# Kernel tuning notes

Measured on AMD Instinct MI355X. Metric: run time of the kernel, lower is better.

Reference implementation:

```python
import jax, jax.numpy as jnp
import numpy as np

NUM_ENTITIES = 100000
NUM_TIMES = 10000
D = 512
DB = 768
NUM_REL = 200
NUM_BASES = 4
N_NODES = 30000
N_EDGES = 200000
B = 128
P_ENT = 64
P_TIME = 32
T_UNIQ = 2000


def setup_inputs() -> dict:
    key = jax.random.key(0)
    ks = jax.random.split(key, 32)
    n = jax.random.normal
    ri = jax.random.randint
    inp = {}
    # learned params
    inp['emb'] = n(ks[0], (NUM_ENTITIES + NUM_TIMES, D), jnp.float32) * 0.05
    sc = 1.0 / np.sqrt(D)
    inp['basis1'] = n(ks[1], (NUM_BASES, D, D), jnp.float32) * sc
    inp['att1'] = n(ks[2], (NUM_REL, NUM_BASES), jnp.float32) * 0.5
    inp['root1'] = n(ks[3], (D, D), jnp.float32) * sc
    inp['bias1'] = jnp.zeros((D,), jnp.float32)
    inp['basis2'] = n(ks[4], (NUM_BASES, D, D), jnp.float32) * sc
    inp['att2'] = n(ks[5], (NUM_REL, NUM_BASES), jnp.float32) * 0.5
    inp['root2'] = n(ks[6], (D, D), jnp.float32) * sc
    inp['bias2'] = jnp.zeros((D,), jnp.float32)
    sb = 1.0 / np.sqrt(DB)
    inp['W_lin'] = n(ks[7], (DB, D), jnp.float32) * sb
    inp['b_lin'] = jnp.zeros((D,), jnp.float32)
    inp['W_attn'] = n(ks[8], (DB, D), jnp.float32) * sb
    inp['b_attn'] = jnp.zeros((D,), jnp.float32)
    inp['W_prob'] = n(ks[9], (DB, 1), jnp.float32) * sb
    inp['b_prob'] = jnp.zeros((1,), jnp.float32)
    # forward tensor args
    inp['ques_emb_bert'] = n(ks[10], (B, DB), jnp.float32)
    inp['x_idx'] = ri(ks[11], (N_NODES,), 0, NUM_ENTITIES, jnp.int32)
    inp['edge_index'] = ri(ks[12], (2, N_EDGES), 0, N_NODES, jnp.int32)
    inp['edge_type'] = ri(ks[13], (N_EDGES,), 0, NUM_REL, jnp.int32)
    inp['start_time'] = ri(ks[14], (N_EDGES,), 0, NUM_TIMES, jnp.int32)
    inp['end_time'] = ri(ks[15], (N_EDGES,), 0, NUM_TIMES, jnp.int32)
    inp['edge_batch_idx'] = jnp.sort(ri(ks[16], (N_EDGES,), 0, B, jnp.int32))
    inp['edge_norm'] = jax.random.uniform(ks[17], (N_EDGES,), jnp.float32)
    inp['uniq_times'] = ri(ks[18], (T_UNIQ,), 0, NUM_TIMES, jnp.int32)
    # padded index vectors: positions >= count point at the appended zero row
    ent_counts = ri(ks[19], (B,), 1, P_ENT + 1, jnp.int32)
    time_counts = ri(ks[20], (B,), 1, P_TIME + 1, jnp.int32)
    pe = ri(ks[21], (B, P_ENT), 0, N_NODES, jnp.int32)
    pt = ri(ks[22], (B, P_TIME), 0, T_UNIQ, jnp.int32)
    inp['padded_ent'] = jnp.where(jnp.arange(P_ENT)[None, :] < ent_counts[:, None], pe, N_NODES)
    inp['padded_time'] = jnp.where(jnp.arange(P_TIME)[None, :] < time_counts[:, None], pt, T_UNIQ)
    inp['ent_counts'] = ent_counts
    inp['time_counts'] = time_counts
    return inp


def rgcn_layer(x, basis, att, root, bias, src, dst, etype, st_emb, et_emb, q_t, edge_norm):
    # basis decomposition: project all nodes through each basis once. [N, NB, D]
    xb = jnp.einsum('ni,bio->nbo', x, basis)
    coeff = att[etype]                                 # [E, NB]
    msg = jnp.einsum('eb,ebd->ed', coeff, xb[src])     # [E, D]
    # time gate: question-time embedding vs edge interval midpoint embedding
    gate = jax.nn.sigmoid(jnp.sum(q_t * 0.5 * (st_emb + et_emb), axis=-1))  # [E]
    msg = msg * (gate * edge_norm)[:, None]
    agg = jax.ops.segment_sum(msg, dst, num_segments=N_NODES)
    return agg + x @ root + bias


def reference(emb, basis1, att1, root1, bias1, basis2, att2, root2, bias2,
              W_lin, b_lin, W_attn, b_attn, W_prob, b_prob,
              ques_emb_bert, x_idx, edge_index, edge_type, start_time, end_time,
              edge_batch_idx, edge_norm, uniq_times, padded_ent, padded_time,
              ent_counts, time_counts):
    question_embedding = ques_emb_bert @ W_lin + b_lin                  # [B, D]
    time_for_edge_attn = (ques_emb_bert @ W_attn + b_attn)[edge_batch_idx]  # [E, D]
    st_emb = emb[start_time + NUM_ENTITIES]
    et_emb = emb[end_time + NUM_ENTITIES]
    x = emb[x_idx]                                                      # [N, D]
    src, dst = edge_index[0], edge_index[1]
    h = jax.nn.relu(rgcn_layer(x, basis1, att1, root1, bias1, src, dst, edge_type,
                               st_emb, et_emb, time_for_edge_attn, edge_norm))
    # dropout is identity in eval mode
    h = rgcn_layer(h, basis2, att2, root2, bias2, src, dst, edge_type,
                   st_emb, et_emb, time_for_edge_attn, edge_norm)       # [N, D]
    subgraph_time_emb = emb[uniq_times + NUM_ENTITIES]                  # [T_u, D]
    zero = jnp.zeros((1, D), h.dtype)
    ent_w_zeros = jnp.concatenate([h, zero], axis=0)
    time_w_zeros = jnp.concatenate([subgraph_time_emb, zero], axis=0)
    pooled_ent = jnp.sum(ent_w_zeros[padded_ent], axis=1) / ent_counts[:, None].astype(h.dtype)
    pooled_time = jnp.sum(time_w_zeros[padded_time], axis=1) / time_counts[:, None].astype(h.dtype)
    p_ent = jax.nn.sigmoid(ques_emb_bert @ W_prob + b_prob)             # [B, 1]
    pred = (question_embedding + pooled_ent * p_ent + pooled_time * (1.0 - p_ent)) / 3.0
    # batched cosine similarity against full entity+time vocab
    pred_n = pred / jnp.maximum(jnp.linalg.norm(pred, axis=-1, keepdims=True), 1e-8)
    emb_n = emb / jnp.maximum(jnp.linalg.norm(emb, axis=-1, keepdims=True), 1e-8)
    score = pred_n @ emb_n.T                                            # [B, V]
    return score * 30.0
```

## Files before the change

kernel.cpp:

```cpp
#include <hip/hip_runtime.h>

#define NUM_ENT   100000
#define NTIMES    10000
#define DD        512
#define DB        768
#define NREL      200
#define NBAS      4
#define NN        30000
#define NEDGE     200000
#define BATCH     128
#define PENT      64
#define PTIME     32
#define TUNIQ     2000
#define V_TOT     110000
#define V_PAD     110208
#define VT16      6888
#define M_PAD2    30208
#define MT2R      1888
#define KT_L      80
#define KT_E      16

typedef __attribute__((ext_vector_type(8))) short s8v;
typedef __attribute__((ext_vector_type(4))) float f4v;

__device__ __forceinline__ unsigned short f2bf(float x){
  unsigned int u = __builtin_bit_cast(unsigned int, x);
  u += 0x7fffu + ((u >> 16) & 1u);
  return (unsigned short)(u >> 16);
}
__device__ __forceinline__ float bf2f(unsigned short h){
  unsigned int u = ((unsigned int)h) << 16;
  return __builtin_bit_cast(float, u);
}

__device__ __forceinline__ void gload16(const void* g, void* l){
  __builtin_amdgcn_global_load_lds(
      (const __attribute__((address_space(1))) void*)g,
      (__attribute__((address_space(3))) void*)l, 16, 0, 0);
}


__global__ __launch_bounds__(256) void k_conv_emb(const float* __restrict__ emb,
    unsigned short* __restrict__ Bp, float* __restrict__ invn){
  int vt = blockIdx.x;
  int wid = threadIdx.x >> 6, lane = threadIdx.x & 63;
  int vrow = vt * 16 + (lane & 15);
  float ss = 0.f;
  __shared__ float ssw[4][16];
  for (int i = 0; i < 4; ++i){
    int kt = wid + i * 4;
    int k0 = kt * 32 + (lane >> 4) * 8;
    s8v o;
    if (vrow < V_TOT){
      const float4* p = reinterpret_cast<const float4*>(emb + (size_t)vrow * DD + k0);
      float4 v0 = p[0], v1 = p[1];
      ss += v0.x*v0.x + v0.y*v0.y + v0.z*v0.z + v0.w*v0.w;
      ss += v1.x*v1.x + v1.y*v1.y + v1.z*v1.z + v1.w*v1.w;
      o[0] = (short)f2bf(v0.x); o[1] = (short)f2bf(v0.y);
      o[2] = (short)f2bf(v0.z); o[3] = (short)f2bf(v0.w);
      o[4] = (short)f2bf(v1.x); o[5] = (short)f2bf(v1.y);
      o[6] = (short)f2bf(v1.z); o[7] = (short)f2bf(v1.w);
    } else {
      #pragma unroll
      for (int j = 0; j < 8; ++j) o[j] = 0;
    }
    *reinterpret_cast<s8v*>(Bp + ((size_t)(kt * VT16 + vt) << 9) + lane * 8) = o;
  }
  ss += __shfl_xor(ss, 16);
  ss += __shfl_xor(ss, 32);
  if ((lane >> 4) == 0) ssw[wid][lane] = ss;
  __syncthreads();
  if (threadIdx.x < 16){
    float s = ssw[0][threadIdx.x] + ssw[1][threadIdx.x] + ssw[2][threadIdx.x] + ssw[3][threadIdx.x];
    int v = vt * 16 + threadIdx.x;
    invn[v] = (v < V_TOT) ? (1.0f / fmaxf(sqrtf(s), 1e-8f)) : 0.0f;
  }
}

__global__ __launch_bounds__(256) void k_small2(const float* __restrict__ ques,
    const float* __restrict__ Wl, const float* __restrict__ bl,
    const float* __restrict__ Wa, const float* __restrict__ ba,
    const float* __restrict__ Wp, const float* __restrict__ bp,
    float* __restrict__ qlin, float* __restrict__ qattn, float* __restrict__ pent){
  if (blockIdx.x == 32){
    int b = threadIdx.x >> 1, half = threadIdx.x & 1;
    float a = 0.f;
    int k0 = half * 384;
    for (int k = k0; k < k0 + 384; ++k)
      a = fmaf(ques[(size_t)b * DB + k], Wp[k], a);
    a += __shfl_xor(a, 1);
    if (half == 0) pent[b] = 1.f / (1.f + expf(-(a + bp[0])));
    return;
  }
  __shared__ float sq[128 * 96];
  int col = threadIdx.x & 31, bg = threadIdx.x >> 5;
  int c0 = blockIdx.x * 32;
  const float* W = (c0 < 512) ? Wl : Wa;
  int wcol = (c0 & 511) + col;
  float acc[16] = {};
  for (int k0 = 0; k0 < DB; k0 += 96){
    __syncthreads();
    for (int i = threadIdx.x; i < 128 * 96; i += 256){
      int b = i / 96, kk = i - b * 96;
      sq[i] = ques[(size_t)b * DB + k0 + kk];
    }
    __syncthreads();
    for (int kk = 0; kk < 96; kk += 4){
      float w0 = W[(size_t)(k0 + kk + 0) * 512 + wcol];
      float w1 = W[(size_t)(k0 + kk + 1) * 512 + wcol];
      float w2 = W[(size_t)(k0 + kk + 2) * 512 + wcol];
      float w3 = W[(size_t)(k0 + kk + 3) * 512 + wcol];
      #pragma unroll
      for (int bb = 0; bb < 16; ++bb){
        float4 qv = *reinterpret_cast<const float4*>(&sq[(bg * 16 + bb) * 96 + kk]);
        acc[bb] = fmaf(qv.x, w0, fmaf(qv.y, w1, fmaf(qv.z, w2, fmaf(qv.w, w3, acc[bb]))));
      }
    }
  }
  float* dst = (c0 < 512) ? qlin : qattn;
  const float* bias = (c0 < 512) ? bl : ba;
  #pragma unroll
  for (int bb = 0; bb < 16; ++bb)
    dst[(size_t)(bg * 16 + bb) * 512 + wcol] = acc[bb] + bias[wcol];
}

__global__ __launch_bounds__(256) void k_pack_qrows(const float* __restrict__ src,
    unsigned short* __restrict__ Ap){
  int w = (int)((blockIdx.x * 256 + threadIdx.x) >> 6);
  int lane = threadIdx.x & 63;
  if (w >= BATCH) return;
  const float* p = src + (size_t)w * 512 + lane * 8;
  s8v o;
  #pragma unroll
  for (int j = 0; j < 8; ++j) o[j] = (short)f2bf(p[j]);
  *reinterpret_cast<s8v*>(Ap + ((size_t)((w >> 4) * KT_E + (lane >> 2)) << 9)
                             + ((w & 15) + (lane & 3) * 16) * 8) = o;
}

__global__ __launch_bounds__(256) void k_pack_B(const float* __restrict__ basis,
    const float* __restrict__ root, unsigned short* __restrict__ Bp){
  int idx = blockIdx.x * 256 + threadIdx.x;
  if (idx >= KT_L * 32 * 64) return;
  int lane = idx & 63; int kt = idx >> 11;
  int k0 = kt * 32 + (lane >> 4) * 8;
  int col = ((idx >> 6) & 31) * 16 + (lane & 15);
  s8v o;
  #pragma unroll
  for (int j = 0; j < 8; ++j){
    int k = k0 + j;
    float v = (k < 2048) ? basis[(size_t)k * 512 + col] : root[(size_t)(k - 2048) * 512 + col];
    o[j] = (short)f2bf(v);
  }
  *reinterpret_cast<s8v*>(Bp + (size_t)idx * 8) = o;
}

__global__ __launch_bounds__(256) void k_gemm_m2(
    const unsigned short* __restrict__ A, const unsigned short* __restrict__ B,
    float* __restrict__ outf){
  __shared__ __align__(1024) short sAll[3 * 8192];
  const int Kt = KT_E;
  int tid = threadIdx.x;
  int lane = tid & 63, wid = tid >> 6;
  int wr = wid >> 1, wc = wid & 1;
  int rt0 = blockIdx.x * 8;
  int ct0 = blockIdx.y * 8;
  const unsigned short* pA0 = A + ((size_t)(rt0 + 2 * wid) * Kt) * 512 + lane * 8;
  const unsigned short* pA1 = pA0 + (size_t)Kt * 512;
  const unsigned short* pB0 = B + (size_t)(ct0 + 2 * wid) * 512 + lane * 8;
  const unsigned short* pB1 = pB0 + 512;
  size_t gbs = (size_t)VT16 * 512;
  int so = 2 * wid * 512;
  f4v acc[4][4] = {};

  auto STAGE = [&](int buf, int kt){
    short* b = &sAll[buf * 8192];
    gload16(pA0 + (size_t)kt * 512, b + so);
    gload16(pA1 + (size_t)kt * 512, b + so + 512);
    gload16(pB0 + (size_t)kt * gbs, b + 4096 + so);
    gload16(pB1 + (size_t)kt * gbs, b + 4096 + so + 512);
  };
  auto COMPUTE = [&](int buf){
    const short* base = &sAll[buf * 8192];
    s8v af[4], bfr[4];
    #pragma unroll
    for (int m = 0; m < 4; ++m) af[m] = *reinterpret_cast<const s8v*>(base + (wr * 4 + m) * 512 + lane * 8);
    #pragma unroll
    for (int n = 0; n < 4; ++n) bfr[n] = *reinterpret_cast<const s8v*>(base + 4096 + (wc * 4 + n) * 512 + lane * 8);
    #pragma unroll
    for (int m = 0; m < 4; ++m)
      #pragma unroll
      for (int n = 0; n < 4; ++n)
        acc[m][n] = __builtin_amdgcn_mfma_f32_16x16x32_bf16(af[m], bfr[n], acc[m][n], 0, 0, 0);
  };

  STAGE(0, 0);
  STAGE(1, 1);
  int cb = 0, sb = 2;
  for (int kt = 0; kt < Kt - 2; ++kt){
    STAGE(sb, kt + 2);
    asm volatile("s_waitcnt vmcnt(8)" ::: "memory");
    __builtin_amdgcn_s_barrier();
    __builtin_amdgcn_sched_barrier(0);
    COMPUTE(cb);
    __builtin_amdgcn_s_barrier();
    cb = (cb == 2) ? 0 : cb + 1;
    sb = (sb == 2) ? 0 : sb + 1;
  }
  asm volatile("s_waitcnt vmcnt(4)" ::: "memory");
  __builtin_amdgcn_s_barrier();
  __builtin_amdgcn_sched_barrier(0);
  COMPUTE(cb);
  cb = (cb == 2) ? 0 : cb + 1;
  asm volatile("s_waitcnt vmcnt(0)" ::: "memory");
  __builtin_amdgcn_s_barrier();
  __builtin_amdgcn_sched_barrier(0);
  COMPUTE(cb);

  #pragma unroll
  for (int m = 0; m < 4; ++m)
    #pragma unroll
    for (int n = 0; n < 4; ++n){
      int row0 = rt0 * 16 + (wr * 4 + m) * 16 + ((lane >> 4) * 4);
      int col  = (ct0 + wc * 4 + n) * 16 + (lane & 15);
      #pragma unroll
      for (int r = 0; r < 4; ++r){
        int rr = row0 + r;
        if (col < NTIMES) outf[(size_t)rr * NTIMES + col] = acc[m][n][r];
      }
    }
}

__global__ __launch_bounds__(256, 3) void k_score_p(
    const unsigned short* __restrict__ Apred, const unsigned short* __restrict__ Bp,
    const float* __restrict__ invn, float* __restrict__ out){
  __shared__ __align__(1024) short sAll[3 * 8192];
  const int Kt = KT_E;
  int tid = threadIdx.x;
  int lane = tid & 63, wid = tid >> 6;
  int wr = wid >> 1, wc = wid & 1;
  int kq = lane >> 4, r16 = lane & 15;
  int ct0 = blockIdx.x * 8;
  const unsigned short* pA0 = Apred + ((size_t)(2 * wid) * Kt) * 512 + lane * 8;
  const unsigned short* pA1 = pA0 + (size_t)Kt * 512;
  const unsigned short* pB0 = Bp + (size_t)(ct0 + 2 * wid) * 512 + lane * 8;
  const unsigned short* pB1 = pB0 + 512;
  size_t gbs = (size_t)VT16 * 512;
  int so = 2 * wid * 512;
  f4v acc[4][4] = {};

  auto STAGE = [&](int buf, int kt){
    short* b = &sAll[buf * 8192];
    gload16(pA0 + (size_t)kt * 512, b + so);
    gload16(pA1 + (size_t)kt * 512, b + so + 512);
    gload16(pB0 + (size_t)kt * gbs, b + 4096 + so);
    gload16(pB1 + (size_t)kt * gbs, b + 4096 + so + 512);
  };
  auto COMPUTE = [&](int buf){
    const short* base = &sAll[buf * 8192];
    s8v af[4], bfr[4];
    #pragma unroll
    for (int m = 0; m < 4; ++m) af[m] = *reinterpret_cast<const s8v*>(base + (wr * 4 + m) * 512 + lane * 8);
    #pragma unroll
    for (int n = 0; n < 4; ++n) bfr[n] = *reinterpret_cast<const s8v*>(base + 4096 + (wc * 4 + n) * 512 + lane * 8);
    #pragma unroll
    for (int m = 0; m < 4; ++m)
      #pragma unroll
      for (int n = 0; n < 4; ++n)
        acc[m][n] = __builtin_amdgcn_mfma_f32_16x16x32_bf16(af[m], bfr[n], acc[m][n], 0, 0, 0);
  };

  STAGE(0, 0);
  STAGE(1, 1);
  int cb = 0, sb = 2;
  for (int kt = 0; kt < Kt - 2; ++kt){
    STAGE(sb, kt + 2);
    asm volatile("s_waitcnt vmcnt(8)" ::: "memory");
    __builtin_amdgcn_s_barrier();
    __builtin_amdgcn_sched_barrier(0);
    COMPUTE(cb);
    __builtin_amdgcn_s_barrier();
    cb = (cb == 2) ? 0 : cb + 1;
    sb = (sb == 2) ? 0 : sb + 1;
  }
  asm volatile("s_waitcnt vmcnt(4)" ::: "memory");
  __builtin_amdgcn_s_barrier();
  __builtin_amdgcn_sched_barrier(0);
  COMPUTE(cb);
  cb = (cb == 2) ? 0 : cb + 1;
  asm volatile("s_waitcnt vmcnt(0)" ::: "memory");
  __builtin_amdgcn_s_barrier();
  __builtin_amdgcn_sched_barrier(0);
  COMPUTE(cb);

  __syncthreads();
  float* scratch = reinterpret_cast<float*>(sAll) + wid * 2176;
  int colg = ct0 * 16 + wc * 64 + r16 * 4;
  bool c_ok = colg < V_TOT;
  float4 inv4 = float4{0.f, 0.f, 0.f, 0.f};
  if (c_ok){
    inv4 = *reinterpret_cast<const float4*>(invn + colg);
    inv4.x *= 30.f; inv4.y *= 30.f; inv4.z *= 30.f; inv4.w *= 30.f;
  }
  #pragma unroll
  for (int p = 0; p < 2; ++p){
    #pragma unroll
    for (int mm = 0; mm < 2; ++mm){
      int m = p * 2 + mm;
      #pragma unroll
      for (int n = 0; n < 4; ++n)
        #pragma unroll
        for (int r = 0; r < 4; ++r)
          scratch[(mm * 16 + kq * 4 + r) * 68 + n * 16 + r16] = acc[m][n][r];
    }
    #pragma unroll
    for (int i = 0; i < 8; ++i){
      int row_r = i * 4 + kq;
      float4 v = *reinterpret_cast<const float4*>(scratch + row_r * 68 + r16 * 4);
      if (c_ok){
        float4 o;
        o.x = v.x * inv4.x; o.y = v.y * inv4.y; o.z = v.z * inv4.z; o.w = v.w * inv4.w;
        int grr = wr * 64 + p * 32 + row_r;
        *reinterpret_cast<float4*>(out + (size_t)grr * V_TOT + colg) = o;
      }
    }
  }
}

template<int MODE>
__global__ __launch_bounds__(512, 4) void k_gemm256(
    const unsigned short* __restrict__ A, const unsigned short* __restrict__ B,
    const float* __restrict__ bias, unsigned short* __restrict__ outh){
  __shared__ __align__(1024) short sAll[3 * 12288];
  const int Kt = KT_L;
  int tid = threadIdx.x;
  int lane = tid & 63, wid = tid >> 6;
  int wr = wid >> 1, wc = wid & 1;
  int g = blockIdx.x;
  int ng = (g & 7) * 59 + (g >> 3);
  int blkM = ng >> 2, blkN = ng & 3;
  int rt0 = blkM * 16;
  int ct0 = blkN * 8;
  const unsigned short* pA0 = A + ((size_t)(rt0 + wid) * Kt) * 512 + lane * 8;
  const unsigned short* pA1 = A + ((size_t)(rt0 + 8 + wid) * Kt) * 512 + lane * 8;
  const unsigned short* pB0 = B + (size_t)(ct0 + wid) * 512 + lane * 8;
  const size_t gbs = 32 * 512;
  int soA0 = wid * 512, soA1 = (8 + wid) * 512, soB = 8192 + wid * 512;
  f4v acc[4][4] = {};

  auto STAGE = [&](int buf, int kt){
    short* b = &sAll[buf * 12288];
    gload16(pA0 + (size_t)kt * 512, b + soA0);
    gload16(pA1 + (size_t)kt * 512, b + soA1);
    gload16(pB0 + (size_t)kt * gbs, b + soB);
  };
  auto COMPUTE = [&](int buf){
    const short* base = &sAll[buf * 12288];
    s8v af[4], bfr[4];
    #pragma unroll
    for (int m = 0; m < 4; ++m) af[m] = *reinterpret_cast<const s8v*>(base + (wr * 4 + m) * 512 + lane * 8);
    #pragma unroll
    for (int n = 0; n < 4; ++n) bfr[n] = *reinterpret_cast<const s8v*>(base + 8192 + (wc * 4 + n) * 512 + lane * 8);
    __builtin_amdgcn_s_setprio(1);
    #pragma unroll
    for (int m = 0; m < 4; ++m)
      #pragma unroll
      for (int n = 0; n < 4; ++n)
        acc[m][n] = __builtin_amdgcn_mfma_f32_16x16x32_bf16(af[m], bfr[n], acc[m][n], 0, 0, 0);
    __builtin_amdgcn_s_setprio(0);
  };

  STAGE(0, 0);
  STAGE(1, 1);
  int cb = 0, sb = 2;
  for (int kt = 0; kt < Kt - 2; ++kt){
    STAGE(sb, kt + 2);
    asm volatile("s_waitcnt vmcnt(6)" ::: "memory");
    __builtin_amdgcn_s_barrier();
    __builtin_amdgcn_sched_barrier(0);
    COMPUTE(cb);
    __builtin_amdgcn_s_barrier();
    cb = (cb == 2) ? 0 : cb + 1;
    sb = (sb == 2) ? 0 : sb + 1;
  }
  asm volatile("s_waitcnt vmcnt(3)" ::: "memory");
  __builtin_amdgcn_s_barrier();
  __builtin_amdgcn_sched_barrier(0);
  COMPUTE(cb);
  cb = (cb == 2) ? 0 : cb + 1;
  asm volatile("s_waitcnt vmcnt(0)" ::: "memory");
  __builtin_amdgcn_s_barrier();
  __builtin_amdgcn_sched_barrier(0);
  COMPUTE(cb);

  int R0 = blkM * 256 + wr * 64 + (lane >> 4) * 4;
  int C0 = blkN * 128 + wc * 64 + (lane & 15);
  #pragma unroll
  for (int m = 0; m < 4; ++m)
    #pragma unroll
    for (int r4 = 0; r4 < 4; ++r4){
      int rr = R0 + m * 16 + r4;
      if (rr < NN){
        #pragma unroll
        for (int n = 0; n < 4; ++n){
          int col = C0 + n * 16;
          float v = acc[m][n][r4] + bias[col];
          if constexpr (MODE == 1) v = fmaxf(v, 0.f);
          outh[(size_t)rr * 512 + col] = f2bf(v);
        }
      }
    }
}

__global__ __launch_bounds__(256) void k_edgeprep(const int* __restrict__ ebatch,
    const int* __restrict__ st, const int* __restrict__ et,
    const float* __restrict__ enorm, const float* __restrict__ M2,
    const int* __restrict__ ei,
    float* __restrict__ we, int* __restrict__ cnt, int* __restrict__ lists){
  int e = blockIdx.x * 256 + threadIdx.x;
  if (e >= NEDGE) return;
  int b = ebatch[e];
  float s = 0.5f * (M2[(size_t)b * NTIMES + st[e]] + M2[(size_t)b * NTIMES + et[e]]);
  we[e] = (1.f / (1.f + expf(-s))) * enorm[e];
  int dst = ei[NEDGE + e];
  int slot = atomicAdd(&cnt[dst], 1);
  if (slot < 64) lists[(size_t)dst * 64 + slot] = e;
}

__global__ __launch_bounds__(256) void k_gather_x(const int* __restrict__ x_idx,
    const float* __restrict__ emb, unsigned short* __restrict__ Ap,
    unsigned short* __restrict__ x_rm){
  int w = (int)((blockIdx.x * 256 + threadIdx.x) >> 6);
  int lane = threadIdx.x & 63;
  if (w >= NN) return;
  int v = x_idx[w];
  const float4* p = reinterpret_cast<const float4*>(emb + (size_t)v * 512 + lane * 8);
  float4 a = p[0], b = p[1];
  s8v x;
  x[0] = (short)f2bf(a.x); x[1] = (short)f2bf(a.y); x[2] = (short)f2bf(a.z); x[3] = (short)f2bf(a.w);
  x[4] = (short)f2bf(b.x); x[5] = (short)f2bf(b.y); x[6] = (short)f2bf(b.z); x[7] = (short)f2bf(b.w);
  *reinterpret_cast<s8v*>(x_rm + (size_t)w * 512 + lane * 8) = x;
  *reinterpret_cast<s8v*>(Ap + ((size_t)(w >> 4) * KT_L + 64 + (lane >> 2)) * 512
                             + ((w & 15) + (lane & 3) * 16) * 8) = x;
}

__global__ __launch_bounds__(256) void k_pack_rows(const unsigned short* __restrict__ src_rm,
    unsigned short* __restrict__ Ap){
  int w = (int)((blockIdx.x * 256 + threadIdx.x) >> 6);
  int lane = threadIdx.x & 63;
  if (w >= NN) return;
  s8v x = *reinterpret_cast<const s8v*>(src_rm + (size_t)w * 512 + lane * 8);
  *reinterpret_cast<s8v*>(Ap + ((size_t)(w >> 4) * KT_L + 64 + (lane >> 2)) * 512
                             + ((w & 15) + (lane & 3) * 16) * 8) = x;
}

__global__ __launch_bounds__(256) void k_edge_agg(const unsigned short* __restrict__ xsrc,
    const int* __restrict__ ei, const int* __restrict__ etype,
    const float* __restrict__ we, const float* __restrict__ att,
    const int* __restrict__ cnt, const int* __restrict__ lists,
    unsigned short* __restrict__ Ap){
  __shared__ float satt[NREL * NBAS];
  __shared__ int sed[4][64];
  for (int i = threadIdx.x; i < NREL * NBAS; i += 256) satt[i] = att[i];
  int wid = threadIdx.x >> 6, lane = threadIdx.x & 63;
  int n = blockIdx.x * 4 + wid;
  int deg = min(cnt[n], 64);
  int eid = (lane < deg) ? lists[(size_t)n * 64 + lane] : 0x7fffffff;
  int rank = 0;
  for (int j = 0; j < 64; ++j){
    int v = __shfl(eid, j);
    rank += (v < eid) ? 1 : 0;
  }
  __syncthreads();
  if (lane < deg) sed[wid][rank] = eid;
  __syncthreads();
  float acc[NBAS][8] = {};
  if (deg > 0){
    int my_e = sed[wid][(lane < deg) ? lane : 0];
    int my_s = ei[my_e];
    int my_t = etype[my_e];
    float my_w = we[my_e];
    float c0l = my_w * satt[my_t * 4 + 0];
    float c1l = my_w * satt[my_t * 4 + 1];
    float c2l = my_w * satt[my_t * 4 + 2];
    float c3l = my_w * satt[my_t * 4 + 3];
    int s0 = __shfl(my_s, 0);
    s8v xv = *reinterpret_cast<const s8v*>(xsrc + (size_t)s0 * 512 + lane * 8);
    for (int j = 0; j < deg; ++j){
      s8v xn = xv;
      if (j + 1 < deg){
        int sn = __shfl(my_s, j + 1);
        xn = *reinterpret_cast<const s8v*>(xsrc + (size_t)sn * 512 + lane * 8);
      }
      float c0 = __shfl(c0l, j), c1 = __shfl(c1l, j);
      float c2 = __shfl(c2l, j), c3 = __shfl(c3l, j);
      #pragma unroll
      for (int jj = 0; jj < 8; ++jj){
        float x = bf2f((unsigned short)xv[jj]);
        acc[0][jj] = fmaf(c0, x, acc[0][jj]);
        acc[1][jj] = fmaf(c1, x, acc[1][jj]);
        acc[2][jj] = fmaf(c2, x, acc[2][jj]);
        acc[3][jj] = fmaf(c3, x, acc[3][jj]);
      }
      xv = xn;
    }
  }
  #pragma unroll
  for (int b = 0; b < NBAS; ++b){
    s8v o;
    #pragma unroll
    for (int jj = 0; jj < 8; ++jj) o[jj] = (short)f2bf(acc[b][jj]);
    *reinterpret_cast<s8v*>(Ap + ((size_t)(n >> 4) * KT_L + b * 16 + (lane >> 2)) * 512
                               + ((n & 15) + (lane & 3) * 16) * 8) = o;
  }
}

__global__ __launch_bounds__(256) void k_pred(const unsigned short* __restrict__ h2,
    const float* __restrict__ emb, const int* __restrict__ uniq,
    const int* __restrict__ pent_idx, const int* __restrict__ ptime_idx,
    const int* __restrict__ ent_c, const int* __restrict__ time_c,
    const float* __restrict__ qlin, const float* __restrict__ pent,
    unsigned short* __restrict__ Ap_pred){
  __shared__ float sacc[4][512];
  int b = blockIdx.x;
  int wid = threadIdx.x >> 6, lane = threadIdx.x & 63;
  float a[8] = {};
  if (wid < 2){
    for (int j = wid * 32; j < wid * 32 + 32; ++j){
      int idx = pent_idx[b * PENT + j];
      if (idx < NN){
        s8v hv = *reinterpret_cast<const s8v*>(h2 + (size_t)idx * 512 + lane * 8);
        #pragma unroll
        for (int jj = 0; jj < 8; ++jj) a[jj] += bf2f((unsigned short)hv[jj]);
      }
    }
  } else {
    for (int j = (wid - 2) * 16; j < (wid - 2) * 16 + 16; ++j){
      int ti = ptime_idx[b * PTIME + j];
      if (ti < TUNIQ){
        const float* p = emb + (size_t)(NUM_ENT + uniq[ti]) * 512 + lane * 8;
        #pragma unroll
        for (int jj = 0; jj < 8; ++jj) a[jj] += p[jj];
      }
    }
  }
  #pragma unroll
  for (int jj = 0; jj < 8; ++jj) sacc[wid][lane * 8 + jj] = a[jj];
  __syncthreads();
  if (wid == 0){
    float ce = 1.f / (float)ent_c[b], ct = 1.f / (float)time_c[b];
    float p = pent[b];
    float pr[8]; float ss = 0.f;
    #pragma unroll
    for (int jj = 0; jj < 8; ++jj){
      int i = lane * 8 + jj;
      float ae = sacc[0][i] + sacc[1][i];
      float at = sacc[2][i] + sacc[3][i];
      float v = (qlin[(size_t)b * 512 + i] + ae * ce * p + at * ct * (1.f - p)) * (1.f / 3.f);
      pr[jj] = v; ss += v * v;
    }
    ss += __shfl_xor(ss, 32); ss += __shfl_xor(ss, 16); ss += __shfl_xor(ss, 8);
    ss += __shfl_xor(ss, 4);  ss += __shfl_xor(ss, 2);  ss += __shfl_xor(ss, 1);
    float inv = 1.f / fmaxf(sqrtf(ss), 1e-8f);
    s8v o;
    #pragma unroll
    for (int jj = 0; jj < 8; ++jj) o[jj] = (short)f2bf(pr[jj] * inv);
    *reinterpret_cast<s8v*>(Ap_pred + ((size_t)((b >> 4) * KT_E + (lane >> 2)) << 9)
                                    + ((b & 15) + (lane & 3) * 16) * 8) = o;
  }
}

extern "C" void kernel_launch(void* const* d_in, const int* in_sizes, int n_in,
                              void* d_out, int out_size, void* d_ws, size_t ws_size,
                              hipStream_t stream){
  const float* emb    = (const float*)d_in[0];
  const float* basis1 = (const float*)d_in[1];
  const float* att1   = (const float*)d_in[2];
  const float* root1  = (const float*)d_in[3];
  const float* bias1  = (const float*)d_in[4];
  const float* basis2 = (const float*)d_in[5];
  const float* att2   = (const float*)d_in[6];
  const float* root2  = (const float*)d_in[7];
  const float* bias2  = (const float*)d_in[8];
  const float* W_lin  = (const float*)d_in[9];
  const float* b_lin  = (const float*)d_in[10];
  const float* W_attn = (const float*)d_in[11];
  const float* b_attn = (const float*)d_in[12];
  const float* W_prob = (const float*)d_in[13];
  const float* b_prob = (const float*)d_in[14];
  const float* ques   = (const float*)d_in[15];
  const int* x_idx    = (const int*)d_in[16];
  const int* eidx     = (const int*)d_in[17];
  const int* etype    = (const int*)d_in[18];
  const int* stime    = (const int*)d_in[19];
  const int* etime    = (const int*)d_in[20];
  const int* ebatch   = (const int*)d_in[21];
  const float* enorm  = (const float*)d_in[22];
  const int* uniq     = (const int*)d_in[23];
  const int* pent_i   = (const int*)d_in[24];
  const int* ptime_i  = (const int*)d_in[25];
  const int* ent_c    = (const int*)d_in[26];
  const int* time_c   = (const int*)d_in[27];
  float* out = (float*)d_out;

  char* w = (char*)d_ws;
  size_t off = 0;
  auto alloc = [&](size_t bytes)->char*{ char* p = w + off; off += (bytes + 255) & ~(size_t)255; return p; };
  unsigned short* Bp_emb = (unsigned short*)alloc((size_t)KT_E * VT16 * 1024);
  float*          invn   = (float*)alloc((size_t)V_PAD * 4);
  unsigned short* Ap   = (unsigned short*)alloc((size_t)MT2R * KT_L * 1024);
  unsigned short* B1p  = (unsigned short*)alloc((size_t)KT_L * 32 * 1024);
  unsigned short* B2p  = (unsigned short*)alloc((size_t)KT_L * 32 * 1024);
  char* xh_base = alloc((size_t)NN * 512 * 2 * 2);
  unsigned short* x_rm = (unsigned short*)xh_base;
  unsigned short* h1   = (unsigned short*)(xh_base + (size_t)NN * 512 * 2);
  unsigned short* h2   = (unsigned short*)xh_base;
  float* M2    = (float*)alloc((size_t)BATCH * NTIMES * 4);
  float* we    = (float*)alloc((size_t)NEDGE * 4);
  float* qlin  = (float*)alloc((size_t)BATCH * 512 * 4);
  float* qattn = (float*)alloc((size_t)BATCH * 512 * 4);
  float* pent  = (float*)alloc(1024);
  unsigned short* Apq    = (unsigned short*)alloc((size_t)8 * KT_E * 1024);
  unsigned short* Appred = (unsigned short*)alloc((size_t)8 * KT_E * 1024);
  int* cnt   = (int*)alloc((size_t)NN * 4);
  int* lists = (int*)alloc((size_t)NN * 64 * 4);
  (void)ws_size; (void)in_sizes; (void)n_in; (void)out_size;

  k_small2<<<33, 256, 0, stream>>>(ques, W_lin, b_lin, W_attn, b_attn, W_prob, b_prob,
                                   qlin, qattn, pent);
  k_pack_qrows<<<32, 256, 0, stream>>>(qattn, Apq);
  k_conv_emb<<<VT16, 256, 0, stream>>>(emb, Bp_emb, invn);
  k_pack_B<<<(KT_L * 32 * 64 + 255) / 256, 256, 0, stream>>>(basis1, root1, B1p);
  k_pack_B<<<(KT_L * 32 * 64 + 255) / 256, 256, 0, stream>>>(basis2, root2, B2p);
  k_gemm_m2<<<dim3(1, 79), 256, 0, stream>>>(Apq, Bp_emb + (size_t)6250 * 512, M2);
  hipMemsetAsync(cnt, 0, (size_t)NN * 4, stream);
  k_edgeprep<<<(NEDGE + 255) / 256, 256, 0, stream>>>(ebatch, stime, etime, enorm, M2,
                                                      eidx, we, cnt, lists);
  k_gather_x<<<NN / 4, 256, 0, stream>>>(x_idx, emb, Ap, x_rm);
  k_edge_agg<<<NN / 4, 256, 0, stream>>>(x_rm, eidx, etype, we, att1, cnt, lists, Ap);
  k_gemm256<1><<<472, 512, 0, stream>>>(Ap, B1p, bias1, h1);
  k_pack_rows<<<NN / 4, 256, 0, stream>>>(h1, Ap);
  k_edge_agg<<<NN / 4, 256, 0, stream>>>(h1, eidx, etype, we, att2, cnt, lists, Ap);
  k_gemm256<2><<<472, 512, 0, stream>>>(Ap, B2p, bias2, h2);
  k_pred<<<BATCH, 256, 0, stream>>>(h2, emb, uniq, pent_i, ptime_i, ent_c, time_c,
                                    qlin, pent, Appred);
  k_score_p<<<861, 256, 0, stream>>>(Appred, Bp_emb, invn, out);
}
```

Before: 685.6 us.

## Widen RGCN GEMM tile to full 512 columns and merge B-packing kernels

The RGCN layer GEMM now gives each 512-thread block 128 rows by all 512 output columns, with each wave computing a 64x128 sub-tile (4x8 MFMAs), instead of 256x128 tiles. The A rows are then loaded from global memory once rather than once per column block, cutting A traffic by a factor of four while raising accumulator register pressure and LDS use per block. Occupancy drops from 4 to 2 blocks per CU, and the grid shrinks to 236 blocks, which roughly matches the CU count. The two weight-packing launches are also merged into a single kernel.

```diff
diff --git a/kernel.cpp b/kernel.cpp
--- a/kernel.cpp
+++ b/kernel.cpp
@@ -137,10 +137,16 @@
                              + ((w & 15) + (lane & 3) * 16) * 8) = o;
 }
 
-__global__ __launch_bounds__(256) void k_pack_B(const float* __restrict__ basis,
-    const float* __restrict__ root, unsigned short* __restrict__ Bp){
+__global__ __launch_bounds__(256) void k_pack_B2(
+    const float* __restrict__ basis1, const float* __restrict__ root1,
+    const float* __restrict__ basis2, const float* __restrict__ root2,
+    unsigned short* __restrict__ B1p, unsigned short* __restrict__ B2p){
   int idx = blockIdx.x * 256 + threadIdx.x;
-  if (idx >= KT_L * 32 * 64) return;
+  int set = idx >= KT_L * 32 * 64;
+  if (set) idx -= KT_L * 32 * 64;
+  const float* basis = set ? basis2 : basis1;
+  const float* root  = set ? root2  : root1;
+  unsigned short* Bp = set ? B2p : B1p;
   int lane = idx & 63; int kt = idx >> 11;
   int k0 = kt * 32 + (lane >> 4) * 8;
   int col = ((idx >> 6) & 31) * 16 + (lane & 15);
@@ -327,44 +333,43 @@
 }
 
 template<int MODE>
-__global__ __launch_bounds__(512, 4) void k_gemm256(
+__global__ __launch_bounds__(512, 2) void k_gemm512(
     const unsigned short* __restrict__ A, const unsigned short* __restrict__ B,
     const float* __restrict__ bias, unsigned short* __restrict__ outh){
-  __shared__ __align__(1024) short sAll[3 * 12288];
+  __shared__ __align__(1024) short sAll[3 * 20480];
   const int Kt = KT_L;
   int tid = threadIdx.x;
   int lane = tid & 63, wid = tid >> 6;
-  int wr = wid >> 1, wc = wid & 1;
-  int g = blockIdx.x;
-  int ng = (g & 7) * 59 + (g >> 3);
-  int blkM = ng >> 2, blkN = ng & 3;
-  int rt0 = blkM * 16;
-  int ct0 = blkN * 8;
-  const unsigned short* pA0 = A + ((size_t)(rt0 + wid) * Kt) * 512 + lane * 8;
-  const unsigned short* pA1 = A + ((size_t)(rt0 + 8 + wid) * Kt) * 512 + lane * 8;
-  const unsigned short* pB0 = B + (size_t)(ct0 + wid) * 512 + lane * 8;
-  const size_t gbs = 32 * 512;
-  int soA0 = wid * 512, soA1 = (8 + wid) * 512, soB = 8192 + wid * 512;
-  f4v acc[4][4] = {};
+  int wr = wid >> 2, wc = wid & 3;
+  int blk = blockIdx.x;
+  int rt0 = blk * 8;
+  const unsigned short* pA = A + ((size_t)(rt0 + wid) * Kt) * 512 + lane * 8;
+  const unsigned short* pB = B + (size_t)(wid * 4) * 512 + lane * 8;
+  int soA = wid * 512;
+  int soB = 4096 + wid * 4 * 512;
+  f4v acc[4][8] = {};
 
   auto STAGE = [&](int buf, int kt){
-    short* b = &sAll[buf * 12288];
-    gload16(pA0 + (size_t)kt * 512, b + soA0);
-    gload16(pA1 + (size_t)kt * 512, b + soA1);
-    gload16(pB0 + (size_t)kt * gbs, b + soB);
+    short* b = &sAll[buf * 20480];
+    gload16(pA + (size_t)kt * 512, b + soA);
+    const unsigned short* pb = pB + (size_t)kt * 32 * 512;
+    gload16(pb,        b + soB);
+    gload16(pb +  512, b + soB +  512);
+    gload16(pb + 1024, b + soB + 1024);
+    gload16(pb + 1536, b + soB + 1536);
   };
   auto COMPUTE = [&](int buf){
-    const short* base = &sAll[buf * 12288];
-    s8v af[4], bfr[4];
+    const short* base = &sAll[buf * 20480];
+    s8v af[4], bfr[8];
     #pragma unroll
     for (int m = 0; m < 4; ++m) af[m] = *reinterpret_cast<const s8v*>(base + (wr * 4 + m) * 512 + lane * 8);
     #pragma unroll
-    for (int n = 0; n < 4; ++n) bfr[n] = *reinterpret_cast<const s8v*>(base + 8192 + (wc * 4 + n) * 512 + lane * 8);
+    for (int n = 0; n < 8; ++n) bfr[n] = *reinterpret_cast<const s8v*>(base + 4096 + (wc * 8 + n) * 512 + lane * 8);
     __builtin_amdgcn_s_setprio(1);
     #pragma unroll
     for (int m = 0; m < 4; ++m)
       #pragma unroll
-      for (int n = 0; n < 4; ++n)
+      for (int n = 0; n < 8; ++n)
         acc[m][n] = __builtin_amdgcn_mfma_f32_16x16x32_bf16(af[m], bfr[n], acc[m][n], 0, 0, 0);
     __builtin_amdgcn_s_setprio(0);
   };
@@ -374,7 +379,7 @@
   int cb = 0, sb = 2;
   for (int kt = 0; kt < Kt - 2; ++kt){
     STAGE(sb, kt + 2);
-    asm volatile("s_waitcnt vmcnt(6)" ::: "memory");
+    asm volatile("s_waitcnt vmcnt(10)" ::: "memory");
     __builtin_amdgcn_s_barrier();
     __builtin_amdgcn_sched_barrier(0);
     COMPUTE(cb);
@@ -382,7 +387,7 @@
     cb = (cb == 2) ? 0 : cb + 1;
     sb = (sb == 2) ? 0 : sb + 1;
   }
-  asm volatile("s_waitcnt vmcnt(3)" ::: "memory");
+  asm volatile("s_waitcnt vmcnt(5)" ::: "memory");
   __builtin_amdgcn_s_barrier();
   __builtin_amdgcn_sched_barrier(0);
   COMPUTE(cb);
@@ -392,8 +397,8 @@
   __builtin_amdgcn_sched_barrier(0);
   COMPUTE(cb);
 
-  int R0 = blkM * 256 + wr * 64 + (lane >> 4) * 4;
-  int C0 = blkN * 128 + wc * 64 + (lane & 15);
+  int R0 = blk * 128 + wr * 64 + ((lane >> 4) * 4);
+  int C0 = wc * 128 + (lane & 15);
   #pragma unroll
   for (int m = 0; m < 4; ++m)
     #pragma unroll
@@ -401,7 +406,7 @@
       int rr = R0 + m * 16 + r4;
       if (rr < NN){
         #pragma unroll
-        for (int n = 0; n < 4; ++n){
+        for (int n = 0; n < 8; ++n){
           int col = C0 + n * 16;
           float v = acc[m][n][r4] + bias[col];
           if constexpr (MODE == 1) v = fmaxf(v, 0.f);
@@ -629,18 +634,18 @@
                                    qlin, qattn, pent);
   k_pack_qrows<<<32, 256, 0, stream>>>(qattn, Apq);
   k_conv_emb<<<VT16, 256, 0, stream>>>(emb, Bp_emb, invn);
-  k_pack_B<<<(KT_L * 32 * 64 + 255) / 256, 256, 0, stream>>>(basis1, root1, B1p);
-  k_pack_B<<<(KT_L * 32 * 64 + 255) / 256, 256, 0, stream>>>(basis2, root2, B2p);
+  k_pack_B2<<<2 * (KT_L * 32 * 64) / 256, 256, 0, stream>>>(basis1, root1, basis2, root2,
+                                                            B1p, B2p);
   k_gemm_m2<<<dim3(1, 79), 256, 0, stream>>>(Apq, Bp_emb + (size_t)6250 * 512, M2);
   hipMemsetAsync(cnt, 0, (size_t)NN * 4, stream);
   k_edgeprep<<<(NEDGE + 255) / 256, 256, 0, stream>>>(ebatch, stime, etime, enorm, M2,
                                                       eidx, we, cnt, lists);
   k_gather_x<<<NN / 4, 256, 0, stream>>>(x_idx, emb, Ap, x_rm);
   k_edge_agg<<<NN / 4, 256, 0, stream>>>(x_rm, eidx, etype, we, att1, cnt, lists, Ap);
-  k_gemm256<1><<<472, 512, 0, stream>>>(Ap, B1p, bias1, h1);
+  k_gemm512<1><<<236, 512, 0, stream>>>(Ap, B1p, bias1, h1);
   k_pack_rows<<<NN / 4, 256, 0, stream>>>(h1, Ap);
   k_edge_agg<<<NN / 4, 256, 0, stream>>>(h1, eidx, etype, we, att2, cnt, lists, Ap);
-  k_gemm256<2><<<472, 512, 0, stream>>>(Ap, B2p, bias2, h2);
+  k_gemm512<2><<<236, 512, 0, stream>>>(Ap, B2p, bias2, h2);
   k_pred<<<BATCH, 256, 0, stream>>>(h2, emb, uniq, pent_i, ptime_i, ent_c, time_c,
                                     qlin, pent, Appred);
   k_score_p<<<861, 256, 0, stream>>>(Appred, Bp_emb, invn, out);
```

Result: no change. 691.7 us (+0.9%).
